# Performance work log

Hardware: AMD Instinct MI355X
Metric: run time of the kernel (lower is better)

The kernel has to match this reference:

```python
import jax, jax.numpy as jnp
import numpy as np

N, E, IN, H, OUT = 100000, 1200000, 128, 64, 2
L = 3          # num GCN layers
EPS = 1e-5     # BatchNorm eps


def setup_inputs() -> dict:
    key = jax.random.key(0)
    ks = jax.random.split(key, 14)
    x = jax.random.normal(ks[0], (N, IN), dtype=jnp.float32)
    edge_index = jax.random.randint(ks[1], (2, E), 0, N, dtype=jnp.int64)
    # GCNConv weights (glorot-ish scale) and biases
    w0 = jax.random.normal(ks[2], (IN, H), dtype=jnp.float32) / np.float32(np.sqrt(IN))
    w1 = jax.random.normal(ks[3], (H, H), dtype=jnp.float32) / np.float32(np.sqrt(H))
    w2 = jax.random.normal(ks[4], (H, H), dtype=jnp.float32) / np.float32(np.sqrt(H))
    biases = jax.random.normal(ks[5], (L, H), dtype=jnp.float32) * 0.01
    # BatchNorm (eval mode): gamma, beta, running mean/var per layer
    gamma = jnp.ones((L, H), jnp.float32) + 0.1 * jax.random.normal(ks[6], (L, H), dtype=jnp.float32)
    beta = 0.1 * jax.random.normal(ks[7], (L, H), dtype=jnp.float32)
    run_mean = 0.1 * jax.random.normal(ks[8], (L, H), dtype=jnp.float32)
    run_var = 0.5 + jax.random.uniform(ks[9], (L, H), dtype=jnp.float32)  # strictly positive
    # classifier
    cls_w = jax.random.normal(ks[10], (H, OUT), dtype=jnp.float32) / np.float32(np.sqrt(H))
    cls_b = jnp.zeros((OUT,), jnp.float32)
    return {"x": x, "edge_index": edge_index, "w0": w0, "w1": w1, "w2": w2,
            "biases": biases, "gamma": gamma, "beta": beta,
            "run_mean": run_mean, "run_var": run_var,
            "cls_w": cls_w, "cls_b": cls_b}


def reference(x, edge_index, w0, w1, w2, biases, gamma, beta, run_mean, run_var, cls_w, cls_b):
    n = x.shape[0]
    loop = jnp.arange(n, dtype=edge_index.dtype)
    row = jnp.concatenate([edge_index[0], loop])  # source (with self-loops)
    col = jnp.concatenate([edge_index[1], loop])  # target (with self-loops)
    # symmetric normalization: D^{-1/2} (A+I) D^{-1/2}, degree on target index
    deg = jax.ops.segment_sum(jnp.ones(row.shape, x.dtype), col, num_segments=n)
    dinv = jnp.where(deg > 0, jax.lax.rsqrt(deg), 0.0)
    norm = dinv[row] * dinv[col]  # [E+N]

    h = x
    for l, w in enumerate((w0, w1, w2)):
        h = h @ w                                                   # [N,H]
        msg = norm[:, None] * h[row]                                # gather + scale [E+N,H]
        h = jax.ops.segment_sum(msg, col, num_segments=n) + biases[l]
        # BatchNorm1d (eval) + ReLU
        scale = gamma[l] * jax.lax.rsqrt(run_var[l] + EPS)
        h = jax.nn.relu((h - run_mean[l]) * scale + beta[l])
        # dropout is identity in eval mode
    return h @ cls_w + cls_b  # [N, OUT]
```

## Files before the change

### kernel.cpp

```cpp
#include <hip/hip_runtime.h>
#include <hip/hip_fp16.h>

#define EPS 1e-5f
#define ABITS 9
#define ACHUNK 4096
#define BCAP 8192
#define BCSR 12288
#define CSHIFT 13
#define NCHUNK 16

typedef _Float16 half8 __attribute__((ext_vector_type(8)));
typedef float floatx4 __attribute__((ext_vector_type(4)));


__global__ __launch_bounds__(256) void bucketA_kernel(const int* __restrict__ ei, int E,
                                                      int* __restrict__ bucket_fill, unsigned* __restrict__ tmp) {
    __shared__ int2 edg[ACHUNK];
    __shared__ int hist[256], lbase[256], lcur[256];
    int t = threadIdx.x;
    hist[t] = 0; lcur[t] = 0;
    __syncthreads();
    int e0 = blockIdx.x * ACHUNK;
    int e1 = e0 + ACHUNK; if (e1 > E) e1 = E;
    int ne = e1 - e0;
    for (int idx = t; idx < ne; idx += 256) {
        int r = ei[e0 + idx], c = ei[E + e0 + idx];
        edg[idx] = make_int2(r, c);
        atomicAdd(&hist[c >> ABITS], 1);
    }
    __syncthreads();
    int h = hist[t];
    if (h) lbase[t] = atomicAdd(&bucket_fill[t], h);
    __syncthreads();
    for (int idx = t; idx < ne; idx += 256) {
        int2 e = edg[idx];
        int b = e.y >> ABITS;
        int l = atomicAdd(&lcur[b], 1);
        tmp[(size_t)b * BCAP + lbase[b] + l] = ((unsigned)(e.y & 511) << 17) | (unsigned)e.x;
    }
}

__global__ __launch_bounds__(256) void bucketB_kernel(const unsigned* __restrict__ tmp,
                                                      const int* __restrict__ bucket_fill,
                                                      int2* __restrict__ rowse, float* __restrict__ dinv,
                                                      int* __restrict__ csr, int n) {
    __shared__ unsigned edg[BCAP];
    __shared__ int cnt2[512 * NCHUNK];
    __shared__ int ps[256];
    int b = blockIdx.x, t = threadIdx.x;
    int n0 = b << ABITS;
    int cntN = n - n0; if (cntN > 512) cntN = 512;
    int ne = bucket_fill[b]; if (ne > BCAP) ne = BCAP;
    int base = b * BCAP;
    int cbase = b * BCSR;
    for (int i = t; i < 512 * NCHUNK; i += 256) cnt2[i] = 0;
    for (int idx = t; idx < ne; idx += 256) edg[idx] = tmp[(size_t)base + idx];
    __syncthreads();
    for (int idx = t; idx < ne; idx += 256) {
        unsigned e = edg[idx];
        int dstOff = e >> 17, src = e & 0x1FFFF;
        atomicAdd(&cnt2[dstOff * NCHUNK + (src >> CSHIFT)], 1);
    }
    __syncthreads();
    int c0 = 0, c1 = 0;
#pragma unroll
    for (int c = 0; c < NCHUNK; ++c) {
        c0 += cnt2[(2 * t) * NCHUNK + c];
        c1 += cnt2[(2 * t + 1) * NCHUNK + c];
    }
    int p0 = (c0 + 7) & ~7, p1 = (c1 + 7) & ~7;
    int s = p0 + p1;
    ps[t] = s;
    __syncthreads();
    for (int off = 1; off < 256; off <<= 1) {
        int u = (t >= off) ? ps[t - off] : 0;
        __syncthreads();
        ps[t] += u;
        __syncthreads();
    }
    int excl = ps[t] - s;
    int st0 = cbase + excl, st1 = cbase + excl + p0;
    if (2 * t < cntN) {
        rowse[n0 + 2 * t] = make_int2(st0, st0 + c0);
        dinv[n0 + 2 * t] = rsqrtf((float)(c0 + 1));
    }
    if (2 * t + 1 < cntN) {
        rowse[n0 + 2 * t + 1] = make_int2(st1, st1 + c1);
        dinv[n0 + 2 * t + 1] = rsqrtf((float)(c1 + 1));
    }
    if (2 * t < cntN)
        for (int j = c0; j < p0; ++j) csr[st0 + j] = n0 + 2 * t;
    if (2 * t + 1 < cntN)
        for (int j = c1; j < p1; ++j) csr[st1 + j] = n0 + 2 * t + 1;
    int run = st0;
#pragma unroll
    for (int c = 0; c < NCHUNK; ++c) {
        int v = cnt2[(2 * t) * NCHUNK + c];
        cnt2[(2 * t) * NCHUNK + c] = run;
        run += v;
    }
    run = st1;
#pragma unroll
    for (int c = 0; c < NCHUNK; ++c) {
        int v = cnt2[(2 * t + 1) * NCHUNK + c];
        cnt2[(2 * t + 1) * NCHUNK + c] = run;
        run += v;
    }
    __syncthreads();
    for (int idx = t; idx < ne; idx += 256) {
        unsigned e = edg[idx];
        int dstOff = e >> 17, src = e & 0x1FFFF;
        int key = dstOff * NCHUNK + (src >> CSHIFT);
        int pos = atomicAdd(&cnt2[key], 1);
        csr[pos] = src;
    }
}


template <int K, typename TIN>
__global__ __launch_bounds__(256) void gemm_kernel(const TIN* __restrict__ A, const float* __restrict__ W,
                                                   const float* __restrict__ dinv, __half* __restrict__ out, int n) {
    const int KP = K + 8;
    __shared__ _Float16 Ah[64 * (K + 8)];
    __shared__ _Float16 Wt[64 * (K + 8)];
    int tid = threadIdx.x;

    for (int idx = tid; idx < K * 64; idx += 256) {
        int k = idx >> 6, c = idx & 63;
        Wt[c * KP + k] = (_Float16)W[idx];
    }
    int row0 = blockIdx.x * 64;
    const TIN* Ab = A + (size_t)row0 * K;
    int limit = (n - row0) * K; if (limit > 64 * K) limit = 64 * K;

    if constexpr (sizeof(TIN) == 4) {
        for (int f = tid * 4; f < 64 * K; f += 1024) {
            float4 v = make_float4(0.f, 0.f, 0.f, 0.f);
            if (f + 3 < limit) {
                v = *(const float4*)((const float*)Ab + f);
            } else {
                if (f + 0 < limit) v.x = ((const float*)Ab)[f + 0];
                if (f + 1 < limit) v.y = ((const float*)Ab)[f + 1];
                if (f + 2 < limit) v.z = ((const float*)Ab)[f + 2];
            }
            int row = f / K, k = f % K;
            _Float16* dst = Ah + row * KP + k;
            dst[0] = (_Float16)v.x; dst[1] = (_Float16)v.y;
            dst[2] = (_Float16)v.z; dst[3] = (_Float16)v.w;
        }
    } else {
        for (int f = tid * 8; f < 64 * K; f += 2048) {
            uint4 v = make_uint4(0, 0, 0, 0);
            if (f + 7 < limit) {
                v = *(const uint4*)((const __half*)Ab + f);
            } else {
                const __half* hp = (const __half*)Ab;
                __half tmp8[8];
                for (int j = 0; j < 8; ++j) tmp8[j] = (f + j < limit) ? hp[f + j] : __half(0);
                v = *(const uint4*)tmp8;
            }
            int row = f / K, k = f % K;
            *(uint4*)(Ah + row * KP + k) = v;
        }
    }
    __syncthreads();

    int w = tid >> 6, lane = tid & 63;
    int m = lane & 15, quad = lane >> 4;
    const _Float16* Aw = Ah + (size_t)(w * 16 + m) * KP + quad * 8;
    const _Float16* Bw = Wt + (size_t)m * KP + quad * 8;

    floatx4 acc0 = {0.f, 0.f, 0.f, 0.f}, acc1 = acc0, acc2 = acc0, acc3 = acc0;
    for (int k0 = 0; k0 < K; k0 += 32) {
        half8 a  = *(const half8*)(Aw + k0);
        half8 b0 = *(const half8*)(Bw + 0 * 16 * KP + k0);
        half8 b1 = *(const half8*)(Bw + 1 * 16 * KP + k0);
        half8 b2 = *(const half8*)(Bw + 2 * 16 * KP + k0);
        half8 b3 = *(const half8*)(Bw + 3 * 16 * KP + k0);
        acc0 = __builtin_amdgcn_mfma_f32_16x16x32_f16(a, b0, acc0, 0, 0, 0);
        acc1 = __builtin_amdgcn_mfma_f32_16x16x32_f16(a, b1, acc1, 0, 0, 0);
        acc2 = __builtin_amdgcn_mfma_f32_16x16x32_f16(a, b2, acc2, 0, 0, 0);
        acc3 = __builtin_amdgcn_mfma_f32_16x16x32_f16(a, b3, acc3, 0, 0, 0);
    }

    int rbase = row0 + w * 16 + quad * 4;
#pragma unroll
    for (int r = 0; r < 4; ++r) {
        int row = rbase + r;
        if (row < n) {
            float dv = dinv[row];
            __half* o = out + (size_t)row * 64 + m;
            o[0]  = __float2half(acc0[r] * dv);
            o[16] = __float2half(acc1[r] * dv);
            o[32] = __float2half(acc2[r] * dv);
            o[48] = __float2half(acc3[r] * dv);
        }
    }
}


__device__ __forceinline__ void agg_add8(float4& lo, float4& hi, uint4 raw) {
    float2 p0 = __half22float2(*(const __half2*)&raw.x);
    float2 p1 = __half22float2(*(const __half2*)&raw.y);
    float2 p2 = __half22float2(*(const __half2*)&raw.z);
    float2 p3 = __half22float2(*(const __half2*)&raw.w);
    lo.x += p0.x; lo.y += p0.y; lo.z += p1.x; lo.w += p1.y;
    hi.x += p2.x; hi.y += p2.y; hi.z += p3.x; hi.w += p3.y;
}

template <bool FUSE_CLS>
__global__ __launch_bounds__(256, 4) void agg_kernel(const __half* __restrict__ t, const float* __restrict__ dinv,
                                                  const int2* __restrict__ rowse, const int* __restrict__ csr,
                                                  const float* __restrict__ bias, const float* __restrict__ gamma,
                                                  const float* __restrict__ beta, const float* __restrict__ mean,
                                                  const float* __restrict__ var, __half* __restrict__ hout,
                                                  float* __restrict__ fout,
                                                  const float* __restrict__ cls_w, const float* __restrict__ cls_b,
                                                  int n) {
    int wave = threadIdx.x >> 6;
    int lane = threadIdx.x & 63;
    int g = lane >> 3;
    int fl = lane & 7;
    int i = (blockIdx.x * (blockDim.x >> 6) + wave) * 8 + g;
    if (i >= n) return;

    uint4 self = *(const uint4*)(t + (size_t)i * 64 + fl * 8);

    float4 lo = make_float4(0.f, 0.f, 0.f, 0.f);
    float4 hi = make_float4(0.f, 0.f, 0.f, 0.f);

    int2 se = rowse[i];
    int deg = se.y - se.x;
    int padEnd = se.x + ((deg + 7) & ~7);
    for (int e = se.x; e < padEnd; e += 8) {
        int s0 = csr[e + 0], s1 = csr[e + 1], s2 = csr[e + 2], s3 = csr[e + 3];
        int s4 = csr[e + 4], s5 = csr[e + 5], s6 = csr[e + 6], s7 = csr[e + 7];
        uint4 r0 = *(const uint4*)(t + (size_t)s0 * 64 + fl * 8);
        uint4 r1 = *(const uint4*)(t + (size_t)s1 * 64 + fl * 8);
        uint4 r2 = *(const uint4*)(t + (size_t)s2 * 64 + fl * 8);
        uint4 r3 = *(const uint4*)(t + (size_t)s3 * 64 + fl * 8);
        uint4 r4 = *(const uint4*)(t + (size_t)s4 * 64 + fl * 8);
        uint4 r5 = *(const uint4*)(t + (size_t)s5 * 64 + fl * 8);
        uint4 r6 = *(const uint4*)(t + (size_t)s6 * 64 + fl * 8);
        uint4 r7 = *(const uint4*)(t + (size_t)s7 * 64 + fl * 8);
        agg_add8(lo, hi, r0); agg_add8(lo, hi, r1); agg_add8(lo, hi, r2); agg_add8(lo, hi, r3);
        agg_add8(lo, hi, r4); agg_add8(lo, hi, r5); agg_add8(lo, hi, r6); agg_add8(lo, hi, r7);
    }

    float coef = 1.0f - (float)(padEnd - se.y);
    {
        float2 p0 = __half22float2(*(const __half2*)&self.x);
        float2 p1 = __half22float2(*(const __half2*)&self.y);
        float2 p2 = __half22float2(*(const __half2*)&self.z);
        float2 p3 = __half22float2(*(const __half2*)&self.w);
        lo.x += coef * p0.x; lo.y += coef * p0.y; lo.z += coef * p1.x; lo.w += coef * p1.y;
        hi.x += coef * p2.x; hi.y += coef * p2.y; hi.z += coef * p3.x; hi.w += coef * p3.y;
    }

    float di = dinv[i];
    lo.x *= di; lo.y *= di; lo.z *= di; lo.w *= di;
    hi.x *= di; hi.y *= di; hi.z *= di; hi.w *= di;

    float4 bbL = ((const float4*)bias)[2 * fl],  bbH = ((const float4*)bias)[2 * fl + 1];
    float4 ggL = ((const float4*)gamma)[2 * fl], ggH = ((const float4*)gamma)[2 * fl + 1];
    float4 beL = ((const float4*)beta)[2 * fl],  beH = ((const float4*)beta)[2 * fl + 1];
    float4 mmL = ((const float4*)mean)[2 * fl],  mmH = ((const float4*)mean)[2 * fl + 1];
    float4 vvL = ((const float4*)var)[2 * fl],   vvH = ((const float4*)var)[2 * fl + 1];
    float4 resL, resH;
    resL.x = fmaxf((lo.x + bbL.x - mmL.x) * (ggL.x * rsqrtf(vvL.x + EPS)) + beL.x, 0.f);
    resL.y = fmaxf((lo.y + bbL.y - mmL.y) * (ggL.y * rsqrtf(vvL.y + EPS)) + beL.y, 0.f);
    resL.z = fmaxf((lo.z + bbL.z - mmL.z) * (ggL.z * rsqrtf(vvL.z + EPS)) + beL.z, 0.f);
    resL.w = fmaxf((lo.w + bbL.w - mmL.w) * (ggL.w * rsqrtf(vvL.w + EPS)) + beL.w, 0.f);
    resH.x = fmaxf((hi.x + bbH.x - mmH.x) * (ggH.x * rsqrtf(vvH.x + EPS)) + beH.x, 0.f);
    resH.y = fmaxf((hi.y + bbH.y - mmH.y) * (ggH.y * rsqrtf(vvH.y + EPS)) + beH.y, 0.f);
    resH.z = fmaxf((hi.z + bbH.z - mmH.z) * (ggH.z * rsqrtf(vvH.z + EPS)) + beH.z, 0.f);
    resH.w = fmaxf((hi.w + bbH.w - mmH.w) * (ggH.w * rsqrtf(vvH.w + EPS)) + beH.w, 0.f);

    if (!FUSE_CLS) {
        __half2 h0 = __floats2half2_rn(resL.x, resL.y);
        __half2 h1 = __floats2half2_rn(resL.z, resL.w);
        __half2 h2 = __floats2half2_rn(resH.x, resH.y);
        __half2 h3 = __floats2half2_rn(resH.z, resH.w);
        uint4 pk;
        pk.x = *(unsigned*)&h0; pk.y = *(unsigned*)&h1;
        pk.z = *(unsigned*)&h2; pk.w = *(unsigned*)&h3;
        ((uint4*)hout)[(size_t)i * 8 + fl] = pk;
    } else {
        const float4* cw = (const float4*)cls_w;
        float4 cwA = cw[4 * fl + 0], cwB = cw[4 * fl + 1], cwC = cw[4 * fl + 2], cwD = cw[4 * fl + 3];
        float c0 = resL.x * cwA.x + resL.y * cwA.z + resL.z * cwB.x + resL.w * cwB.z
                 + resH.x * cwC.x + resH.y * cwC.z + resH.z * cwD.x + resH.w * cwD.z;
        float c1 = resL.x * cwA.y + resL.y * cwA.w + resL.z * cwB.y + resL.w * cwB.w
                 + resH.x * cwC.y + resH.y * cwC.w + resH.z * cwD.y + resH.w * cwD.w;
        for (int off = 4; off > 0; off >>= 1) {
            c0 += __shfl_xor(c0, off);
            c1 += __shfl_xor(c1, off);
        }
        if (fl == 0) {
            fout[(size_t)i * 2 + 0] = c0 + cls_b[0];
            fout[(size_t)i * 2 + 1] = c1 + cls_b[1];
        }
    }
}


extern "C" void kernel_launch(void* const* d_in, const int* in_sizes, int n_in,
                              void* d_out, int out_size, void* d_ws, size_t ws_size,
                              hipStream_t stream) {
    const float* x      = (const float*)d_in[0];
    const int*   ei     = (const int*)d_in[1];
    const float* w0     = (const float*)d_in[2];
    const float* w1     = (const float*)d_in[3];
    const float* w2     = (const float*)d_in[4];
    const float* biases = (const float*)d_in[5];
    const float* gamma  = (const float*)d_in[6];
    const float* beta   = (const float*)d_in[7];
    const float* rmean  = (const float*)d_in[8];
    const float* rvar   = (const float*)d_in[9];
    const float* cls_w  = (const float*)d_in[10];
    const float* cls_b  = (const float*)d_in[11];
    float* out = (float*)d_out;

    const int IN = 128, H = 64;
    const int N = in_sizes[0] / IN;
    const int E = in_sizes[1] / 2;

    char* p = (char*)d_ws;
    auto carve = [&](size_t bytes) { void* q = (void*)p; p += (bytes + 255) & ~(size_t)255; return q; };
    float* dinv    = (float*)carve((size_t)N * 4);
    int2*  rowse   = (int2*)carve((size_t)N * 8);
    int*   bucket_fill = (int*)carve((size_t)256 * 4);
    unsigned* tmp  = (unsigned*)carve((size_t)256 * BCAP * 4);
    int*   csr     = (int*)carve((size_t)256 * BCSR * 4);
    __half* tbuf   = (__half*)carve((size_t)N * H * 2);
    __half* hbuf   = (__half*)carve((size_t)N * H * 2);

    int nbuckets = (N + (1 << ABITS) - 1) >> ABITS;
    int na = (E + ACHUNK - 1) / ACHUNK;

    hipMemsetAsync(bucket_fill, 0, (size_t)256 * 4, stream);
    bucketA_kernel<<<na, 256, 0, stream>>>(ei, E, bucket_fill, tmp);
    bucketB_kernel<<<nbuckets, 256, 0, stream>>>(tmp, bucket_fill, rowse, dinv, csr, N);

    int gemm_grid = (N + 63) / 64;
    int agg_grid  = (N + 31) / 32;

    gemm_kernel<128, float><<<gemm_grid, 256, 0, stream>>>(x, w0, dinv, tbuf, N);
    agg_kernel<false><<<agg_grid, 256, 0, stream>>>(tbuf, dinv, rowse, csr,
        biases + 0, gamma + 0, beta + 0, rmean + 0, rvar + 0, hbuf, nullptr, nullptr, nullptr, N);
    gemm_kernel<64, __half><<<gemm_grid, 256, 0, stream>>>(hbuf, w1, dinv, tbuf, N);
    agg_kernel<false><<<agg_grid, 256, 0, stream>>>(tbuf, dinv, rowse, csr,
        biases + H, gamma + H, beta + H, rmean + H, rvar + H, hbuf, nullptr, nullptr, nullptr, N);
    gemm_kernel<64, __half><<<gemm_grid, 256, 0, stream>>>(hbuf, w2, dinv, tbuf, N);
    agg_kernel<true><<<agg_grid, 256, 0, stream>>>(tbuf, dinv, rowse, csr,
        biases + 2 * H, gamma + 2 * H, beta + 2 * H, rmean + 2 * H, rvar + 2 * H, nullptr, out, cls_w, cls_b, N);
}
```

Before: 251.3 us.

## Fuse aggregation with next-layer GEMM and process nodes in degree-sorted order

New measurement: 243.0 us. 3.3% less time.

```diff
diff --git a/kernel.cpp b/kernel.cpp
--- a/kernel.cpp
+++ b/kernel.cpp
@@ -43,16 +43,18 @@
 __global__ __launch_bounds__(256) void bucketB_kernel(const unsigned* __restrict__ tmp,
                                                       const int* __restrict__ bucket_fill,
                                                       int2* __restrict__ rowse, float* __restrict__ dinv,
-                                                      int* __restrict__ csr, int n) {
+                                                      int* __restrict__ csr, int* __restrict__ classCnt, int n) {
     __shared__ unsigned edg[BCAP];
     __shared__ int cnt2[512 * NCHUNK];
     __shared__ int ps[256];
+    __shared__ int ccnt[16];
     int b = blockIdx.x, t = threadIdx.x;
     int n0 = b << ABITS;
     int cntN = n - n0; if (cntN > 512) cntN = 512;
     int ne = bucket_fill[b]; if (ne > BCAP) ne = BCAP;
     int base = b * BCAP;
     int cbase = b * BCSR;
+    if (t < 16) ccnt[t] = 0;
     for (int i = t; i < 512 * NCHUNK; i += 256) cnt2[i] = 0;
     for (int idx = t; idx < ne; idx += 256) edg[idx] = tmp[(size_t)base + idx];
     __syncthreads();
@@ -67,6 +69,12 @@
     for (int c = 0; c < NCHUNK; ++c) {
         c0 += cnt2[(2 * t) * NCHUNK + c];
         c1 += cnt2[(2 * t + 1) * NCHUNK + c];
+    }
+    {
+        int k0c = (c0 + 7) >> 3; if (k0c > 15) k0c = 15;
+        int k1c = (c1 + 7) >> 3; if (k1c > 15) k1c = 15;
+        if (2 * t < cntN) atomicAdd(&ccnt[k0c], 1);
+        if (2 * t + 1 < cntN) atomicAdd(&ccnt[k1c], 1);
     }
     int p0 = (c0 + 7) & ~7, p1 = (c1 + 7) & ~7;
     int s = p0 + p1;
@@ -114,6 +122,35 @@
         int pos = atomicAdd(&cnt2[key], 1);
         csr[pos] = src;
     }
+    __syncthreads();
+    if (t < 16) atomicAdd(&classCnt[t], ccnt[t]);
+}
+
+__global__ __launch_bounds__(256) void perm_kernel(const int2* __restrict__ rowse,
+                                                   const int* __restrict__ classCnt,
+                                                   int* __restrict__ classCur,
+                                                   int* __restrict__ perm, int n) {
+    __shared__ int lcnt[16], lbase[16], gbase[16];
+    int t = threadIdx.x;
+    if (t < 16) lcnt[t] = 0;
+    __syncthreads();
+    int i = blockIdx.x * 256 + t;
+    int k = 0, lrank = 0;
+    if (i < n) {
+        int2 se = rowse[i];
+        int deg = se.y - se.x;
+        k = (deg + 7) >> 3; if (k > 15) k = 15;
+        lrank = atomicAdd(&lcnt[k], 1);
+    }
+    __syncthreads();
+    if (t < 16) {
+        lbase[t] = atomicAdd(&classCur[t], lcnt[t]);
+        int bsum = 0;
+        for (int j = 0; j < t; ++j) bsum += classCnt[j];
+        gbase[t] = bsum;
+    }
+    __syncthreads();
+    if (i < n) perm[gbase[k] + lbase[k] + lrank] = i;
 }
 
 
@@ -208,22 +245,12 @@
     hi.x += p2.x; hi.y += p2.y; hi.z += p3.x; hi.w += p3.y;
 }
 
-template <bool FUSE_CLS>
-__global__ __launch_bounds__(256, 4) void agg_kernel(const __half* __restrict__ t, const float* __restrict__ dinv,
-                                                  const int2* __restrict__ rowse, const int* __restrict__ csr,
-                                                  const float* __restrict__ bias, const float* __restrict__ gamma,
-                                                  const float* __restrict__ beta, const float* __restrict__ mean,
-                                                  const float* __restrict__ var, __half* __restrict__ hout,
-                                                  float* __restrict__ fout,
-                                                  const float* __restrict__ cls_w, const float* __restrict__ cls_b,
-                                                  int n) {
-    int wave = threadIdx.x >> 6;
-    int lane = threadIdx.x & 63;
-    int g = lane >> 3;
-    int fl = lane & 7;
-    int i = (blockIdx.x * (blockDim.x >> 6) + wave) * 8 + g;
-    if (i >= n) return;
-
+__device__ __forceinline__ void agg_core(const __half* __restrict__ t, const float* __restrict__ dinv,
+                                         const int2* __restrict__ rowse, const int* __restrict__ csr,
+                                         const float* __restrict__ bias, const float* __restrict__ gamma,
+                                         const float* __restrict__ beta, const float* __restrict__ mean,
+                                         const float* __restrict__ var,
+                                         int i, int fl, float4& resL, float4& resH, float& di) {
     uint4 self = *(const uint4*)(t + (size_t)i * 64 + fl * 8);
 
     float4 lo = make_float4(0.f, 0.f, 0.f, 0.f);
@@ -257,7 +284,7 @@
         hi.x += coef * p2.x; hi.y += coef * p2.y; hi.z += coef * p3.x; hi.w += coef * p3.y;
     }
 
-    float di = dinv[i];
+    di = dinv[i];
     lo.x *= di; lo.y *= di; lo.z *= di; lo.w *= di;
     hi.x *= di; hi.y *= di; hi.z *= di; hi.w *= di;
 
@@ -266,7 +293,6 @@
     float4 beL = ((const float4*)beta)[2 * fl],  beH = ((const float4*)beta)[2 * fl + 1];
     float4 mmL = ((const float4*)mean)[2 * fl],  mmH = ((const float4*)mean)[2 * fl + 1];
     float4 vvL = ((const float4*)var)[2 * fl],   vvH = ((const float4*)var)[2 * fl + 1];
-    float4 resL, resH;
     resL.x = fmaxf((lo.x + bbL.x - mmL.x) * (ggL.x * rsqrtf(vvL.x + EPS)) + beL.x, 0.f);
     resL.y = fmaxf((lo.y + bbL.y - mmL.y) * (ggL.y * rsqrtf(vvL.y + EPS)) + beL.y, 0.f);
     resL.z = fmaxf((lo.z + bbL.z - mmL.z) * (ggL.z * rsqrtf(vvL.z + EPS)) + beL.z, 0.f);
@@ -275,8 +301,39 @@
     resH.y = fmaxf((hi.y + bbH.y - mmH.y) * (ggH.y * rsqrtf(vvH.y + EPS)) + beH.y, 0.f);
     resH.z = fmaxf((hi.z + bbH.z - mmH.z) * (ggH.z * rsqrtf(vvH.z + EPS)) + beH.z, 0.f);
     resH.w = fmaxf((hi.w + bbH.w - mmH.w) * (ggH.w * rsqrtf(vvH.w + EPS)) + beH.w, 0.f);
-
-    if (!FUSE_CLS) {
+}
+
+__global__ __launch_bounds__(256, 4) void agg_gemm_kernel(
+        const __half* __restrict__ t, const float* __restrict__ dinv,
+        const int2* __restrict__ rowse, const int* __restrict__ csr,
+        const int* __restrict__ perm,
+        const float* __restrict__ bias, const float* __restrict__ gamma,
+        const float* __restrict__ beta, const float* __restrict__ mean,
+        const float* __restrict__ var,
+        const float* __restrict__ W,
+        __half* __restrict__ tout, int n) {
+    const int KP = 72;
+    __shared__ _Float16 Ah[32 * 72];
+    __shared__ _Float16 Wt[64 * 72];
+    __shared__ int   nidS[32];
+    __shared__ float dvS[32];
+
+    int tid = threadIdx.x;
+    for (int idx = tid; idx < 64 * 64; idx += 256) {
+        int k = idx >> 6, c = idx & 63;
+        Wt[c * KP + k] = (_Float16)W[idx];
+    }
+
+    int wave = tid >> 6, lane = tid & 63;
+    int g = lane >> 3, fl = lane & 7;
+    int slotInBlk = wave * 8 + g;
+    int slot = blockIdx.x * 32 + slotInBlk;
+    bool act = slot < n;
+
+    if (act) {
+        int i = perm[slot];
+        float4 resL, resH; float di;
+        agg_core(t, dinv, rowse, csr, bias, gamma, beta, mean, var, i, fl, resL, resH, di);
         __half2 h0 = __floats2half2_rn(resL.x, resL.y);
         __half2 h1 = __floats2half2_rn(resL.z, resL.w);
         __half2 h2 = __floats2half2_rn(resH.x, resH.y);
@@ -284,22 +341,78 @@
         uint4 pk;
         pk.x = *(unsigned*)&h0; pk.y = *(unsigned*)&h1;
         pk.z = *(unsigned*)&h2; pk.w = *(unsigned*)&h3;
-        ((uint4*)hout)[(size_t)i * 8 + fl] = pk;
+        *(uint4*)(Ah + slotInBlk * KP + fl * 8) = pk;
+        if (fl == 0) { nidS[slotInBlk] = i; dvS[slotInBlk] = di; }
     } else {
-        const float4* cw = (const float4*)cls_w;
-        float4 cwA = cw[4 * fl + 0], cwB = cw[4 * fl + 1], cwC = cw[4 * fl + 2], cwD = cw[4 * fl + 3];
-        float c0 = resL.x * cwA.x + resL.y * cwA.z + resL.z * cwB.x + resL.w * cwB.z
-                 + resH.x * cwC.x + resH.y * cwC.z + resH.z * cwD.x + resH.w * cwD.z;
-        float c1 = resL.x * cwA.y + resL.y * cwA.w + resL.z * cwB.y + resL.w * cwB.w
-                 + resH.x * cwC.y + resH.y * cwC.w + resH.z * cwD.y + resH.w * cwD.w;
-        for (int off = 4; off > 0; off >>= 1) {
-            c0 += __shfl_xor(c0, off);
-            c1 += __shfl_xor(c1, off);
+        uint4 z = make_uint4(0, 0, 0, 0);
+        *(uint4*)(Ah + slotInBlk * KP + fl * 8) = z;
+        if (fl == 0) { nidS[slotInBlk] = 0; dvS[slotInBlk] = 0.f; }
+    }
+    __syncthreads();
+
+    int m = lane & 15, quad = lane >> 4;
+    int mrow = (wave & 1) * 16;
+    int c0 = (wave >> 1) * 32;
+    const _Float16* Aw = Ah + (mrow + m) * KP + quad * 8;
+    const _Float16* Bw = Wt + (c0 + m) * KP + quad * 8;
+
+    floatx4 acc0 = {0.f, 0.f, 0.f, 0.f}, acc1 = acc0;
+#pragma unroll
+    for (int k0 = 0; k0 < 64; k0 += 32) {
+        half8 a  = *(const half8*)(Aw + k0);
+        half8 b0 = *(const half8*)(Bw + k0);
+        half8 b1 = *(const half8*)(Bw + 16 * KP + k0);
+        acc0 = __builtin_amdgcn_mfma_f32_16x16x32_f16(a, b0, acc0, 0, 0, 0);
+        acc1 = __builtin_amdgcn_mfma_f32_16x16x32_f16(a, b1, acc1, 0, 0, 0);
+    }
+
+#pragma unroll
+    for (int r = 0; r < 4; ++r) {
+        int row = mrow + quad * 4 + r;
+        if (blockIdx.x * 32 + row < n) {
+            int node = nidS[row];
+            float dv = dvS[row];
+            __half* o = tout + (size_t)node * 64;
+            o[c0 + m]      = __float2half(acc0[r] * dv);
+            o[c0 + 16 + m] = __float2half(acc1[r] * dv);
         }
-        if (fl == 0) {
-            fout[(size_t)i * 2 + 0] = c0 + cls_b[0];
-            fout[(size_t)i * 2 + 1] = c1 + cls_b[1];
-        }
+    }
+}
+
+__global__ __launch_bounds__(256, 4) void agg_cls_kernel(
+        const __half* __restrict__ t, const float* __restrict__ dinv,
+        const int2* __restrict__ rowse, const int* __restrict__ csr,
+        const int* __restrict__ perm,
+        const float* __restrict__ bias, const float* __restrict__ gamma,
+        const float* __restrict__ beta, const float* __restrict__ mean,
+        const float* __restrict__ var,
+        float* __restrict__ fout,
+        const float* __restrict__ cls_w, const float* __restrict__ cls_b,
+        int n) {
+    int wave = threadIdx.x >> 6;
+    int lane = threadIdx.x & 63;
+    int g = lane >> 3;
+    int fl = lane & 7;
+    int slot = (blockIdx.x * (blockDim.x >> 6) + wave) * 8 + g;
+    if (slot >= n) return;
+    int i = perm[slot];
+
+    float4 resL, resH; float di;
+    agg_core(t, dinv, rowse, csr, bias, gamma, beta, mean, var, i, fl, resL, resH, di);
+
+    const float4* cw = (const float4*)cls_w;
+    float4 cwA = cw[4 * fl + 0], cwB = cw[4 * fl + 1], cwC = cw[4 * fl + 2], cwD = cw[4 * fl + 3];
+    float c0 = resL.x * cwA.x + resL.y * cwA.z + resL.z * cwB.x + resL.w * cwB.z
+             + resH.x * cwC.x + resH.y * cwC.z + resH.z * cwD.x + resH.w * cwD.z;
+    float c1 = resL.x * cwA.y + resL.y * cwA.w + resL.z * cwB.y + resL.w * cwB.w
+             + resH.x * cwC.y + resH.y * cwC.w + resH.z * cwD.y + resH.w * cwD.w;
+    for (int off = 4; off > 0; off >>= 1) {
+        c0 += __shfl_xor(c0, off);
+        c1 += __shfl_xor(c1, off);
+    }
+    if (fl == 0) {
+        fout[(size_t)i * 2 + 0] = c0 + cls_b[0];
+        fout[(size_t)i * 2 + 1] = c1 + cls_b[1];
     }
 }
 
@@ -329,29 +442,34 @@
     auto carve = [&](size_t bytes) { void* q = (void*)p; p += (bytes + 255) & ~(size_t)255; return q; };
     float* dinv    = (float*)carve((size_t)N * 4);
     int2*  rowse   = (int2*)carve((size_t)N * 8);
-    int*   bucket_fill = (int*)carve((size_t)256 * 4);
+    int*   meta    = (int*)carve((size_t)288 * 4);
+    int*   perm    = (int*)carve((size_t)N * 4);
     unsigned* tmp  = (unsigned*)carve((size_t)256 * BCAP * 4);
     int*   csr     = (int*)carve((size_t)256 * BCSR * 4);
-    __half* tbuf   = (__half*)carve((size_t)N * H * 2);
-    __half* hbuf   = (__half*)carve((size_t)N * H * 2);
+    __half* tA     = (__half*)carve((size_t)N * H * 2);
+    __half* tB     = (__half*)carve((size_t)N * H * 2);
+
+    int* bucket_fill = meta;
+    int* classCnt    = meta + 256;
+    int* classCur    = meta + 272;
 
     int nbuckets = (N + (1 << ABITS) - 1) >> ABITS;
     int na = (E + ACHUNK - 1) / ACHUNK;
 
-    hipMemsetAsync(bucket_fill, 0, (size_t)256 * 4, stream);
+    hipMemsetAsync(meta, 0, (size_t)288 * 4, stream);
     bucketA_kernel<<<na, 256, 0, stream>>>(ei, E, bucket_fill, tmp);
-    bucketB_kernel<<<nbuckets, 256, 0, stream>>>(tmp, bucket_fill, rowse, dinv, csr, N);
+    bucketB_kernel<<<nbuckets, 256, 0, stream>>>(tmp, bucket_fill, rowse, dinv, csr, classCnt, N);
+    perm_kernel<<<(N + 255) / 256, 256, 0, stream>>>(rowse, classCnt, classCur, perm, N);
 
     int gemm_grid = (N + 63) / 64;
     int agg_grid  = (N + 31) / 32;
 
-    gemm_kernel<128, float><<<gemm_grid, 256, 0, stream>>>(x, w0, dinv, tbuf, N);
-    agg_kernel<false><<<agg_grid, 256, 0, stream>>>(tbuf, dinv, rowse, csr,
-        biases + 0, gamma + 0, beta + 0, rmean + 0, rvar + 0, hbuf, nullptr, nullptr, nullptr, N);
-    gemm_kernel<64, __half><<<gemm_grid, 256, 0, stream>>>(hbuf, w1, dinv, tbuf, N);
-    agg_kernel<false><<<agg_grid, 256, 0, stream>>>(tbuf, dinv, rowse, csr,
-        biases + H, gamma + H, beta + H, rmean + H, rvar + H, hbuf, nullptr, nullptr, nullptr, N);
-    gemm_kernel<64, __half><<<gemm_grid, 256, 0, stream>>>(hbuf, w2, dinv, tbuf, N);
-    agg_kernel<true><<<agg_grid, 256, 0, stream>>>(tbuf, dinv, rowse, csr,
-        biases + 2 * H, gamma + 2 * H, beta + 2 * H, rmean + 2 * H, rvar + 2 * H, nullptr, out, cls_w, cls_b, N);
-}
+    gemm_kernel<128, float><<<gemm_grid, 256, 0, stream>>>(x, w0, dinv, tA, N);
+    agg_gemm_kernel<<<agg_grid, 256, 0, stream>>>(tA, dinv, rowse, csr, perm,
+        biases + 0, gamma + 0, beta + 0, rmean + 0, rvar + 0, w1, tB, N);
+    agg_gemm_kernel<<<agg_grid, 256, 0, stream>>>(tB, dinv, rowse, csr, perm,
+        biases + H, gamma + H, beta + H, rmean + H, rvar + H, w2, tA, N);
+    agg_cls_kernel<<<agg_grid, 256, 0, stream>>>(tA, dinv, rowse, csr, perm,
+        biases + 2 * H, gamma + 2 * H, beta + 2 * H, rmean + 2 * H, rvar + 2 * H,
+        out, cls_w, cls_b, N);
+}
```
